# Performance work log

Measured on AMD Instinct MI355X. Metric: run time of the kernel, lower is better.

Reference implementation:

```python
import jax, jax.numpy as jnp
import numpy as np

B, N, M, C1, C2 = 4, 8192, 2048, 128, 256
H1, H2 = 256, 128  # mlp = [C2+C1, 256, 128]
EPS_DIST = 1e-8
EPS_BN = 1e-5
K = 3


def setup_inputs() -> dict:
    key = jax.random.key(0)
    ks = jax.random.split(key, 6)
    return {
        "unknown": jax.random.normal(ks[0], (B, N, 3), dtype=jnp.float32),
        "known": jax.random.normal(ks[1], (B, M, 3), dtype=jnp.float32),
        "unknow_feats": jax.random.normal(ks[2], (B, C1, N), dtype=jnp.float32),
        "known_feats": jax.random.normal(ks[3], (B, C2, M), dtype=jnp.float32),
        "W1": jax.random.normal(ks[4], (H1, C1 + C2), dtype=jnp.float32) * 0.05,
        "g1": jnp.ones((H1,), jnp.float32),
        "b1": jnp.zeros((H1,), jnp.float32),
        "W2": jax.random.normal(ks[5], (H2, H1), dtype=jnp.float32) * 0.05,
        "g2": jnp.ones((H2,), jnp.float32),
        "b2": jnp.zeros((H2,), jnp.float32),
    }


def _bn_relu(x, g, b):
    # training-mode BatchNorm over (batch, spatial) axes for (B, C, N) tensor
    mean = jnp.mean(x, axis=(0, 2), keepdims=True)
    var = jnp.var(x, axis=(0, 2), keepdims=True)
    y = (x - mean) * jax.lax.rsqrt(var + EPS_BN) * g[None, :, None] + b[None, :, None]
    return jax.nn.relu(y)


def reference(unknown, known, unknow_feats, known_feats, W1, g1, b1, W2, g2, b2):
    # 3-NN: squared euclidean distances (B, N, M) via expansion (avoids B,N,M,3 temp)
    d2 = (
        jnp.sum(unknown * unknown, axis=-1)[:, :, None]
        + jnp.sum(known * known, axis=-1)[:, None, :]
        - 2.0 * jnp.einsum("bnc,bmc->bnm", unknown, known)
    )
    neg_d, idx = jax.lax.top_k(-d2, K)  # smallest-K squared dists
    dist = -neg_d  # (B, N, K), squared distances (pytorch3d knn_points convention)
    recip = 1.0 / (dist + EPS_DIST)
    weight = recip / jnp.sum(recip, axis=2, keepdims=True)  # (B, N, K)

    kf = jnp.swapaxes(known_feats, 1, 2)  # (B, M, C2)
    grouped = jax.vmap(lambda f, i: f[i])(kf, idx)  # (B, N, K, C2)
    interp = jnp.einsum("bnkc,bnk->bcn", grouped, weight)  # (B, C2, N)

    x = jnp.concatenate([interp, unknow_feats], axis=1)  # (B, C2+C1, N)
    x = _bn_relu(jnp.einsum("oc,bcn->bon", W1, x), g1, b1)
    x = _bn_relu(jnp.einsum("oc,bcn->bon", W2, x), g2, b2)
    return x  # (B, H2, N)
```

## Files before the change

kernel.cpp:

```cpp
#include <hip/hip_runtime.h>
#include <hip/hip_bf16.h>
#include <cstdint>
#include <cstddef>

typedef unsigned short u16;
typedef __attribute__((ext_vector_type(8))) short bf16x8;
typedef __attribute__((ext_vector_type(4))) float f32x4;

constexpr int Bn = 4;
constexpr int Nq = 8192;
constexpr int Mk = 2048;
constexpr int C1c = 128;
constexpr int C2c = 256;
constexpr int H1c = 256;
constexpr int H2c = 128;

__device__ __forceinline__ float bf2f(u16 u) {
    union { uint32_t i; float f; } v;
    v.i = (uint32_t)u << 16;
    return v.f;
}
__device__ __forceinline__ u16 f2bf(float f) {
    const uint32_t x = __float_as_uint(f);
    return (u16)((x + 0x7FFFu + ((x >> 16) & 1u)) >> 16);
}
__device__ __forceinline__ uint32_t cvtpk(float lo, float hi) {
    uint32_t r;
    asm("v_cvt_pk_bf16_f32 %0, %1, %2" : "=v"(r) : "v"(lo), "v"(hi));
    return r;
}

__global__ __launch_bounds__(256) void knn_prep_kernel(
    const float* __restrict__ W1, const float* __restrict__ W2,
    u16* __restrict__ W1b, u16* __restrict__ W2b,
    const float* __restrict__ KF, u16* __restrict__ KFt,
    const float* __restrict__ UF, u16* __restrict__ UFt,
    const float* __restrict__ unknown, const float* __restrict__ known,
    int* __restrict__ idx_out, float* __restrict__ w_out)
{
    __shared__ __align__(16) char smem[32768];
    const int bid = blockIdx.x;
    const int t = threadIdx.x;

    if (bid < 1024) {
        float4* kp = (float4*)smem;
        const int b = bid >> 8;
        const int n0 = (bid & 255) * 32;

        const float* kb = known + (size_t)b * Mk * 3;
        for (int i = t; i < Mk; i += 256) {
            const float x = kb[i * 3 + 0], y = kb[i * 3 + 1], z = kb[i * 3 + 2];
            kp[i] = make_float4(x, y, z, fmaf(x, x, fmaf(y, y, z * z)));
        }
        __syncthreads();

        const int q = n0 + (t >> 3);
        const int s = t & 7;
        const float* u = unknown + ((size_t)b * Nq + q) * 3;
        const float ux = u[0], uy = u[1], uz = u[2];
        const float nux = -2.0f * ux, nuy = -2.0f * uy, nuz = -2.0f * uz;
        const float uu = fmaf(ux, ux, fmaf(uy, uy, uz * uz));

        float d0 = 1e30f, d1 = 1e30f, d2 = 1e30f;
        int i0 = 0, i1 = 0, i2 = 0;

        auto ins = [&](float d, int i) {
            const bool c0 = d < d0, c1 = d < d1, c2 = d < d2;
            const float nd0 = fminf(d0, d);
            const float nd1 = __builtin_amdgcn_fmed3f(d0, d, d1);
            const float nd2 = __builtin_amdgcn_fmed3f(d1, d, d2);
            i2 = c1 ? i1 : (c2 ? i : i2);
            i1 = c0 ? i0 : (c1 ? i : i1);
            i0 = c0 ? i : i0;
            d0 = nd0; d1 = nd1; d2 = nd2;
        };

        #pragma unroll 8
        for (int it = 0; it < Mk / 8; ++it) {
            const int m = it * 8 + s;
            const float4 p = kp[m];
            const float d = fmaf(nux, p.x, fmaf(nuy, p.y, fmaf(nuz, p.z, p.w)));
            ins(d, m);
        }
        #pragma unroll
        for (int off = 1; off <= 4; off <<= 1) {
            const float e0 = __shfl_xor(d0, off), e1 = __shfl_xor(d1, off), e2 = __shfl_xor(d2, off);
            const int j0 = __shfl_xor(i0, off), j1 = __shfl_xor(i1, off), j2 = __shfl_xor(i2, off);
            ins(e0, j0);
            ins(e1, j1);
            ins(e2, j2);
        }
        if (s == 0) {
            const float f0 = d0 + uu, f1 = d1 + uu, f2 = d2 + uu;
            const float r0 = 1.0f / (f0 + 1e-8f);
            const float r1 = 1.0f / (f1 + 1e-8f);
            const float r2 = 1.0f / (f2 + 1e-8f);
            const float inv = 1.0f / (r0 + r1 + r2);
            const size_t base = ((size_t)b * Nq + q) * 3;
            idx_out[base + 0] = i0;
            idx_out[base + 1] = i1;
            idx_out[base + 2] = i2;
            w_out[base + 0] = r0 * inv;
            w_out[base + 1] = r1 * inv;
            w_out[base + 2] = r2 * inv;
        }
    } else if (bid < 1152) {
        const int cb = bid - 1024;
        const float* X = (cb < 96) ? W1 : W2;
        u16* Y = (cb < 96) ? W1b : W2b;
        const int i = ((cb < 96) ? cb : (cb - 96)) * 256 + t;
        const float4 v = *(const float4*)&X[(size_t)i * 4];
        ushort4 o;
        o.x = f2bf(v.x); o.y = f2bf(v.y); o.z = f2bf(v.z); o.w = f2bf(v.w);
        *(ushort4*)&Y[(size_t)i * 4] = o;
    } else {
        const float* X;
        u16* Y;
        int C, M, m0, c0;
        if (bid < 1664) {
            const int f = bid - 1152;
            const int b = f >> 7, rem = f & 127;
            C = C2c; M = Mk; m0 = (rem >> 2) * 64; c0 = (rem & 3) * 64;
            X = KF + (size_t)b * C * M;
            Y = KFt + (size_t)b * M * C;
        } else {
            const int f = bid - 1664;
            const int b = f >> 8, rem = f & 255;
            C = C1c; M = Nq; m0 = (rem >> 1) * 64; c0 = (rem & 1) * 64;
            X = UF + (size_t)b * C * M;
            Y = UFt + (size_t)b * M * C;
        }
        float (*T)[65] = (float(*)[65])smem;
        const int m4 = (t & 15) * 4, cr = t >> 4;
        #pragma unroll
        for (int i = 0; i < 4; ++i) {
            const float4 v = *(const float4*)&X[(size_t)(c0 + cr + i * 16) * M + m0 + m4];
            T[cr + i * 16][m4 + 0] = v.x;
            T[cr + i * 16][m4 + 1] = v.y;
            T[cr + i * 16][m4 + 2] = v.z;
            T[cr + i * 16][m4 + 3] = v.w;
        }
        __syncthreads();
        const int c4 = (t & 15) * 4, mr = t >> 4;
        #pragma unroll
        for (int i = 0; i < 4; ++i) {
            const int m = mr + i * 16;
            ushort4 o;
            o.x = f2bf(T[c4 + 0][m]);
            o.y = f2bf(T[c4 + 1][m]);
            o.z = f2bf(T[c4 + 2][m]);
            o.w = f2bf(T[c4 + 3][m]);
            *(ushort4*)&Y[(size_t)(m0 + m) * C + c0 + c4] = o;
        }
    }
}

__device__ __forceinline__ uint4 bnx(uint4 x, const float* scs, const float* bis, int k) {
    const u16* p = (const u16*)&x;
    const float4 s0 = *(const float4*)&scs[k];
    const float4 s1 = *(const float4*)&scs[k + 4];
    const float4 b0 = *(const float4*)&bis[k];
    const float4 b1 = *(const float4*)&bis[k + 4];
    const float* sa = (const float*)&s0;
    const float* sb = (const float*)&s1;
    const float* ba = (const float*)&b0;
    const float* bb = (const float*)&b1;
    uint4 o;
    uint32_t* po = (uint32_t*)&o;
    #pragma unroll
    for (int w2 = 0; w2 < 2; ++w2) {
        const float a0 = fmaxf(0.0f, fmaf(bf2f(p[2 * w2 + 0]), sa[2 * w2 + 0], ba[2 * w2 + 0]));
        const float a1 = fmaxf(0.0f, fmaf(bf2f(p[2 * w2 + 1]), sa[2 * w2 + 1], ba[2 * w2 + 1]));
        po[w2] = cvtpk(a0, a1);
    }
    #pragma unroll
    for (int w2 = 0; w2 < 2; ++w2) {
        const float a0 = fmaxf(0.0f, fmaf(bf2f(p[4 + 2 * w2 + 0]), sb[2 * w2 + 0], bb[2 * w2 + 0]));
        const float a1 = fmaxf(0.0f, fmaf(bf2f(p[4 + 2 * w2 + 1]), sb[2 * w2 + 1], bb[2 * w2 + 1]));
        po[2 + w2] = cvtpk(a0, a1);
    }
    return o;
}

template <int GATHER, int STATS>
__global__ __launch_bounds__(256) void mfma_gemm(
    const u16* __restrict__ A, int lda, size_t sA,
    const u16* __restrict__ Bt, int ldb, size_t sB,
    u16* __restrict__ Cout, int ldc, size_t sC,
    int nK,
    const u16* __restrict__ Ptb,
    const int* __restrict__ idx, const float* __restrict__ wgt, int nrows,
    float* __restrict__ partS, float* __restrict__ partQ)
{
    __shared__ u16 As[4096];
    __shared__ u16 Bs[4096];
    __shared__ float sS[2][128], sQ[2][128];

    const int b = blockIdx.z;
    const int m0 = blockIdx.x * 128, n0 = blockIdx.y * 128;
    const int t = threadIdx.x;
    const int l = t & 63, wv = t >> 6;
    const int wr = wv >> 1, wc = wv & 1;

    const u16* Ab = A + (size_t)b * sA;
    const u16* Btb = Bt + (size_t)b * sB;
    const int rA0 = t >> 2, rA1 = (t + 256) >> 2;
    const int ko = (t & 3) * 8;

    f32x4 acc[4][4];
    const f32x4 z = {0.0f, 0.0f, 0.0f, 0.0f};
    #pragma unroll
    for (int i = 0; i < 4; ++i)
        #pragma unroll
        for (int j = 0; j < 4; ++j) acc[i][j] = z;

    uint4 a0 = *(const uint4*)&Ab[(size_t)(m0 + rA0) * lda + ko];
    uint4 a1 = *(const uint4*)&Ab[(size_t)(m0 + rA1) * lda + ko];
    uint4 b0 = *(const uint4*)&Btb[(size_t)(n0 + rA0) * ldb + ko];
    uint4 b1 = *(const uint4*)&Btb[(size_t)(n0 + rA1) * ldb + ko];

    for (int kt = 0; kt < nK; ++kt) {
        *(uint4*)&As[t * 8] = a0;
        *(uint4*)&As[(t + 256) * 8] = a1;
        *(uint4*)&Bs[t * 8] = b0;
        *(uint4*)&Bs[(t + 256) * 8] = b1;
        __syncthreads();
        if (kt + 1 < nK) {
            const int k0 = (kt + 1) * 32;
            a0 = *(const uint4*)&Ab[(size_t)(m0 + rA0) * lda + k0 + ko];
            a1 = *(const uint4*)&Ab[(size_t)(m0 + rA1) * lda + k0 + ko];
            b0 = *(const uint4*)&Btb[(size_t)(n0 + rA0) * ldb + k0 + ko];
            b1 = *(const uint4*)&Btb[(size_t)(n0 + rA1) * ldb + k0 + ko];
        }
        bf16x8 af[4], bf[4];
        #pragma unroll
        for (int f = 0; f < 4; ++f) {
            af[f] = *(const bf16x8*)&As[(wr * 64 + f * 16 + (l & 15)) * 32 + (l >> 4) * 8];
            bf[f] = *(const bf16x8*)&Bs[(wc * 64 + f * 16 + (l & 15)) * 32 + (l >> 4) * 8];
        }
        #pragma unroll
        for (int i = 0; i < 4; ++i)
            #pragma unroll
            for (int j = 0; j < 4; ++j)
                acc[i][j] = __builtin_amdgcn_mfma_f32_16x16x32_bf16(af[i], bf[j], acc[i][j], 0, 0, 0);
        __syncthreads();
    }

    const int cb = l & 15;
    const int rg = (l >> 4) * 4;
    float sj[4] = {0, 0, 0, 0}, qj[4] = {0, 0, 0, 0};
    #pragma unroll
    for (int i = 0; i < 4; ++i) {
        #pragma unroll
        for (int r = 0; r < 4; ++r) {
            const int R = m0 + wr * 64 + i * 16 + rg + r;
            const u16 *P0 = nullptr, *P1 = nullptr, *P2 = nullptr;
            float w0 = 0.0f, w1 = 0.0f, w2 = 0.0f;
            if (GATHER) {
                const size_t ib = ((size_t)b * nrows + R) * 3;
                const int j0 = idx[ib], j1 = idx[ib + 1], j2 = idx[ib + 2];
                w0 = wgt[ib];
                w1 = wgt[ib + 1];
                w2 = wgt[ib + 2];
                const u16* Pb = Ptb + (size_t)b * Mk * 256;
                P0 = Pb + (size_t)j0 * 256;
                P1 = Pb + (size_t)j1 * 256;
                P2 = Pb + (size_t)j2 * 256;
            }
            #pragma unroll
            for (int j = 0; j < 4; ++j) {
                const int Cc = n0 + wc * 64 + j * 16 + cb;
                float v = acc[i][j][r];
                if (GATHER)
                    v += w0 * bf2f(P0[Cc]) + w1 * bf2f(P1[Cc]) + w2 * bf2f(P2[Cc]);
                Cout[(size_t)b * sC + (size_t)R * ldc + Cc] = f2bf(v);
                if (STATS) {
                    sj[j] += v;
                    qj[j] += v * v;
                }
            }
        }
    }

    if (STATS) {
        #pragma unroll
        for (int j = 0; j < 4; ++j) {
            float s = sj[j], q = qj[j];
            s += __shfl_xor(s, 16); s += __shfl_xor(s, 32);
            q += __shfl_xor(q, 16); q += __shfl_xor(q, 32);
            if (l < 16) {
                sS[wr][wc * 64 + j * 16 + l] = s;
                sQ[wr][wc * 64 + j * 16 + l] = q;
            }
        }
        __syncthreads();
        if (t < 128) {
            const float S = sS[0][t] + sS[1][t];
            const float Q = sQ[0][t] + sQ[1][t];
            const int pblk = blockIdx.z * gridDim.x + blockIdx.x;
            partS[(size_t)pblk * 256 + blockIdx.y * 128 + t] = S;
            partQ[(size_t)pblk * 256 + blockIdx.y * 128 + t] = Q;
        }
    }
}

__global__ __launch_bounds__(256) void mfma_gemm3(
    const u16* __restrict__ W2b,
    const u16* __restrict__ Y,
    float* __restrict__ out,
    const float* __restrict__ bn_s, const float* __restrict__ bn_b,
    float* __restrict__ partS, float* __restrict__ partQ)
{
    __shared__ u16 As[2048];
    __shared__ u16 Bs[4096];
    __shared__ float scs[256], bis[256];
    __shared__ float sS[2][64], sQ[2][64];

    const int b = blockIdx.z;
    const int m0 = blockIdx.x * 64;
    const int n0 = blockIdx.y * 128;
    const int t = threadIdx.x;
    const int l = t & 63, wv = t >> 6;
    const int wr = wv >> 1, wc = wv & 1;

    scs[t] = bn_s[t];
    bis[t] = bn_b[t];

    const u16* Yb = Y + (size_t)b * Nq * 256;
    const int rA = t >> 2;
    const int rB1 = (t + 256) >> 2;
    const int ko = (t & 3) * 8;

    f32x4 acc[2][4];
    const f32x4 z = {0.0f, 0.0f, 0.0f, 0.0f};
    #pragma unroll
    for (int i = 0; i < 2; ++i)
        #pragma unroll
        for (int j = 0; j < 4; ++j) acc[i][j] = z;

    uint4 a0 = *(const uint4*)&W2b[(size_t)(m0 + rA) * 256 + ko];
    uint4 b0 = *(const uint4*)&Yb[(size_t)(n0 + rA) * 256 + ko];
    uint4 b1 = *(const uint4*)&Yb[(size_t)(n0 + rB1) * 256 + ko];
    __syncthreads();

    for (int kt = 0; kt < 8; ++kt) {
        const int k = kt * 32 + ko;
        *(uint4*)&As[t * 8] = a0;
        *(uint4*)&Bs[t * 8] = bnx(b0, scs, bis, k);
        *(uint4*)&Bs[(t + 256) * 8] = bnx(b1, scs, bis, k);
        __syncthreads();
        if (kt + 1 < 8) {
            const int k0 = (kt + 1) * 32;
            a0 = *(const uint4*)&W2b[(size_t)(m0 + rA) * 256 + k0 + ko];
            b0 = *(const uint4*)&Yb[(size_t)(n0 + rA) * 256 + k0 + ko];
            b1 = *(const uint4*)&Yb[(size_t)(n0 + rB1) * 256 + k0 + ko];
        }
        bf16x8 af[2], bf[4];
        #pragma unroll
        for (int f = 0; f < 2; ++f)
            af[f] = *(const bf16x8*)&As[(wr * 32 + f * 16 + (l & 15)) * 32 + (l >> 4) * 8];
        #pragma unroll
        for (int f = 0; f < 4; ++f)
            bf[f] = *(const bf16x8*)&Bs[(wc * 64 + f * 16 + (l & 15)) * 32 + (l >> 4) * 8];
        #pragma unroll
        for (int i = 0; i < 2; ++i)
            #pragma unroll
            for (int j = 0; j < 4; ++j)
                acc[i][j] = __builtin_amdgcn_mfma_f32_16x16x32_bf16(af[i], bf[j], acc[i][j], 0, 0, 0);
        __syncthreads();
    }

    const int cb = l & 15;
    const int rg = (l >> 4) * 4;
    float* ob = out + (size_t)b * H2c * Nq;
    #pragma unroll
    for (int i = 0; i < 2; ++i) {
        #pragma unroll
        for (int r = 0; r < 4; ++r) {
            const int Rl = wr * 32 + i * 16 + rg + r;
            #pragma unroll
            for (int j = 0; j < 4; ++j) {
                const int Cc = n0 + wc * 64 + j * 16 + cb;
                ob[(size_t)(m0 + Rl) * Nq + Cc] = acc[i][j][r];
            }
            float s = acc[i][0][r] + acc[i][1][r] + acc[i][2][r] + acc[i][3][r];
            float q = acc[i][0][r] * acc[i][0][r] + acc[i][1][r] * acc[i][1][r] +
                      acc[i][2][r] * acc[i][2][r] + acc[i][3][r] * acc[i][3][r];
            s += __shfl_xor(s, 1); s += __shfl_xor(s, 2);
            s += __shfl_xor(s, 4); s += __shfl_xor(s, 8);
            q += __shfl_xor(q, 1); q += __shfl_xor(q, 2);
            q += __shfl_xor(q, 4); q += __shfl_xor(q, 8);
            if ((l & 15) == 0) {
                sS[wc][Rl] = s;
                sQ[wc][Rl] = q;
            }
        }
    }
    __syncthreads();
    if (t < 64) {
        const float S = sS[0][t] + sS[1][t];
        const float Q = sQ[0][t] + sQ[1][t];
        const int p = blockIdx.z * gridDim.y + blockIdx.y;
        partS[(size_t)p * 128 + m0 + t] = S;
        partQ[(size_t)p * 128 + m0 + t] = Q;
    }
}

__global__ __launch_bounds__(1024) void bn_finalize(
    const float* __restrict__ pS, const float* __restrict__ pQ,
    const float* __restrict__ g, const float* __restrict__ beta,
    float* __restrict__ scale, float* __restrict__ bias,
    int C, int np, float cnt)
{
    __shared__ float rs[1024], rq[1024];
    const int t = threadIdx.x;
    const int c = t & (C - 1);
    const int sl = t / C;
    const int nsl = 1024 / C;
    float s = 0.0f, q = 0.0f;
    for (int i = sl; i < np; i += nsl) {
        s += pS[(size_t)i * C + c];
        q += pQ[(size_t)i * C + c];
    }
    rs[t] = s;
    rq[t] = q;
    __syncthreads();
    if (t < C) {
        for (int k = 1; k < nsl; ++k) {
            s += rs[t + k * C];
            q += rq[t + k * C];
        }
        const float mean = s / cnt;
        const float var = q / cnt - mean * mean;
        const float r = rsqrtf(var + 1e-5f);
        const float sc = g[t] * r;
        scale[t] = sc;
        bias[t] = beta[t] - mean * sc;
    }
}

__global__ __launch_bounds__(256) void bn2_apply_kernel(
    float* __restrict__ Y,
    const float* __restrict__ pS, const float* __restrict__ pQ,
    const float* __restrict__ g, const float* __restrict__ beta)
{
    __shared__ float rs[256], rq[256];
    const int t = threadIdx.x;
    const size_t base = (size_t)blockIdx.x * 1024;
    const int c = (int)((base / Nq) % H2c);

    rs[t] = pS[(size_t)t * 128 + c];
    rq[t] = pQ[(size_t)t * 128 + c];
    __syncthreads();
    for (int off = 128; off > 0; off >>= 1) {
        if (t < off) {
            rs[t] += rs[t + off];
            rq[t] += rq[t + off];
        }
        __syncthreads();
    }
    if (t == 0) {
        const float cnt = (float)(Bn * Nq);
        const float mean = rs[0] / cnt;
        const float var = rq[0] / cnt - mean * mean;
        const float r = rsqrtf(var + 1e-5f);
        const float sc = g[c] * r;
        rs[0] = sc;
        rq[0] = beta[c] - mean * sc;
    }
    __syncthreads();
    const float sc = rs[0], bi = rq[0];
    float4 v = *(float4*)&Y[base + t * 4];
    v.x = fmaxf(0.0f, fmaf(v.x, sc, bi));
    v.y = fmaxf(0.0f, fmaf(v.y, sc, bi));
    v.z = fmaxf(0.0f, fmaf(v.z, sc, bi));
    v.w = fmaxf(0.0f, fmaf(v.w, sc, bi));
    *(float4*)&Y[base + t * 4] = v;
}

extern "C" void kernel_launch(void* const* d_in, const int* in_sizes, int n_in,
                              void* d_out, int out_size, void* d_ws, size_t ws_size,
                              hipStream_t stream) {
    const float* unknown = (const float*)d_in[0];
    const float* known = (const float*)d_in[1];
    const float* unknow_feats = (const float*)d_in[2];
    const float* known_feats = (const float*)d_in[3];
    const float* W1 = (const float*)d_in[4];
    const float* g1 = (const float*)d_in[5];
    const float* b1 = (const float*)d_in[6];
    const float* W2 = (const float*)d_in[7];
    const float* g2 = (const float*)d_in[8];
    const float* b2 = (const float*)d_in[9];
    float* out = (float*)d_out;

    char* w = (char*)d_ws;
    u16* KFt = (u16*)w; w += (size_t)Bn * Mk * C2c * 2;
    u16* UFt = (u16*)w; w += (size_t)Bn * Nq * C1c * 2;
    u16* W1b = (u16*)w; w += (size_t)H1c * 384 * 2;
    u16* W2b = (u16*)w; w += (size_t)H2c * H1c * 2;
    u16* Ptb = (u16*)w; w += (size_t)Bn * Mk * H1c * 2;
    u16* y1b = (u16*)w; w += (size_t)Bn * Nq * H1c * 2;
    int* idx = (int*)w; w += (size_t)Bn * Nq * 3 * 4;
    float* wgt = (float*)w; w += (size_t)Bn * Nq * 3 * 4;
    float* pS1 = (float*)w; w += (size_t)256 * 256 * 4;
    float* pQ1 = (float*)w; w += (size_t)256 * 256 * 4;
    float* pS2 = (float*)w; w += (size_t)256 * 128 * 4;
    float* pQ2 = (float*)w; w += (size_t)256 * 128 * 4;
    float* scale1 = (float*)w; w += 1024;
    float* bias1 = (float*)w; w += 1024;

    knn_prep_kernel<<<2688, 256, 0, stream>>>(W1, W2, W1b, W2b,
                                              known_feats, KFt, unknow_feats, UFt,
                                              unknown, known, idx, wgt);

    mfma_gemm<0, 0><<<dim3(Mk / 128, H1c / 128, Bn), 256, 0, stream>>>(
        KFt, C2c, (size_t)Mk * C2c,
        W1b, 384, 0,
        Ptb, H1c, (size_t)Mk * H1c,
        C2c / 32, nullptr, nullptr, nullptr, 0, nullptr, nullptr);

    mfma_gemm<1, 1><<<dim3(Nq / 128, H1c / 128, Bn), 256, 0, stream>>>(
        UFt, C1c, (size_t)Nq * C1c,
        W1b + C2c, 384, 0,
        y1b, H1c, (size_t)Nq * H1c,
        C1c / 32, Ptb, idx, wgt, Nq, pS1, pQ1);

    bn_finalize<<<1, 1024, 0, stream>>>(pS1, pQ1, g1, b1, scale1, bias1,
                                        H1c, 256, (float)(Bn * Nq));

    mfma_gemm3<<<dim3(2, Nq / 128, Bn), 256, 0, stream>>>(
        W2b, y1b, out, scale1, bias1, pS2, pQ2);

    bn2_apply_kernel<<<(Bn * H2c * Nq) / 1024, 256, 0, stream>>>(out, pS2, pQ2, g2, b2);
}
```

Baseline: 104.8 us.

## Fuse known-feature projection GEMM into prep kernel and BN1 finalize into GEMM2

The known-feature GEMM (KF^T times W1[:, :256]) now runs inside the prep kernel: each block reads fp32 known_feats and W1, converts them to bf16 while staging in LDS, and writes the projected Ptb directly. This removes the KFt transpose buffer and one kernel launch. The BN1 finalize kernel is also removed. The last block of the second GEMM, detected with an atomic counter, reduces the partial sums and writes scale/bias. Launch count and intermediate traffic go down, at the cost of a smaller 64x64 MFMA tile with no overlap between loads and MMA, and a serial 256-step reduction in a single block.

Result: slower. 166.7 us (+59.0%).

```diff
diff --git a/kernel.cpp b/kernel.cpp
--- a/kernel.cpp
+++ b/kernel.cpp
@@ -33,10 +33,11 @@
 __global__ __launch_bounds__(256) void knn_prep_kernel(
     const float* __restrict__ W1, const float* __restrict__ W2,
     u16* __restrict__ W1b, u16* __restrict__ W2b,
-    const float* __restrict__ KF, u16* __restrict__ KFt,
+    const float* __restrict__ KF, u16* __restrict__ Ptb,
     const float* __restrict__ UF, u16* __restrict__ UFt,
     const float* __restrict__ unknown, const float* __restrict__ known,
-    int* __restrict__ idx_out, float* __restrict__ w_out)
+    int* __restrict__ idx_out, float* __restrict__ w_out,
+    int* __restrict__ done1)
 {
     __shared__ __align__(16) char smem[32768];
     const int bid = blockIdx.x;
@@ -105,6 +106,7 @@
             w_out[base + 2] = r2 * inv;
         }
     } else if (bid < 1152) {
+        if (bid == 1024 && t == 0) *done1 = 0;
         const int cb = bid - 1024;
         const float* X = (cb < 96) ? W1 : W2;
         u16* Y = (cb < 96) ? W1b : W2b;
@@ -113,28 +115,88 @@
         ushort4 o;
         o.x = f2bf(v.x); o.y = f2bf(v.y); o.z = f2bf(v.z); o.w = f2bf(v.w);
         *(ushort4*)&Y[(size_t)i * 4] = o;
+    } else if (bid < 1664) {
+        u16* As = (u16*)smem;
+        u16* Bs = (u16*)(smem + 5120);
+        const int f = bid - 1152;
+        const int b = f >> 7;
+        const int rem = f & 127;
+        const int m0 = (rem >> 2) * 64;
+        const int h0 = (rem & 3) * 64;
+        const float* KFb = KF + (size_t)b * C2c * Mk;
+        const int l = t & 63, wv = t >> 6;
+        const int wr = wv >> 1, wc = wv & 1;
+
+        f32x4 acc[2][2];
+        const f32x4 z = {0.0f, 0.0f, 0.0f, 0.0f};
+        acc[0][0] = z; acc[0][1] = z; acc[1][0] = z; acc[1][1] = z;
+
+        const int cA = t >> 3;
+        const int mcA = (t & 7) * 8;
+        const int hB = t >> 2;
+        const int khB = (t & 3) * 8;
+
+        for (int kt = 0; kt < 8; ++kt) {
+            const int kc = kt * 32;
+            {
+                const float* src = &KFb[(size_t)(kc + cA) * Mk + m0 + mcA];
+                const float4 v0 = *(const float4*)&src[0];
+                const float4 v1 = *(const float4*)&src[4];
+                As[(mcA + 0) * 40 + cA] = f2bf(v0.x);
+                As[(mcA + 1) * 40 + cA] = f2bf(v0.y);
+                As[(mcA + 2) * 40 + cA] = f2bf(v0.z);
+                As[(mcA + 3) * 40 + cA] = f2bf(v0.w);
+                As[(mcA + 4) * 40 + cA] = f2bf(v1.x);
+                As[(mcA + 5) * 40 + cA] = f2bf(v1.y);
+                As[(mcA + 6) * 40 + cA] = f2bf(v1.z);
+                As[(mcA + 7) * 40 + cA] = f2bf(v1.w);
+            }
+            {
+                const float* src = &W1[(size_t)(h0 + hB) * 384 + kc + khB];
+                const float4 v0 = *(const float4*)&src[0];
+                const float4 v1 = *(const float4*)&src[4];
+                u16 o[8] = {f2bf(v0.x), f2bf(v0.y), f2bf(v0.z), f2bf(v0.w),
+                            f2bf(v1.x), f2bf(v1.y), f2bf(v1.z), f2bf(v1.w)};
+                *(uint4*)&Bs[hB * 40 + khB] = *(const uint4*)o;
+            }
+            __syncthreads();
+            bf16x8 af[2], bf[2];
+            #pragma unroll
+            for (int ff = 0; ff < 2; ++ff) {
+                af[ff] = *(const bf16x8*)&As[(wr * 32 + ff * 16 + (l & 15)) * 40 + (l >> 4) * 8];
+                bf[ff] = *(const bf16x8*)&Bs[(wc * 32 + ff * 16 + (l & 15)) * 40 + (l >> 4) * 8];
+            }
+            #pragma unroll
+            for (int i = 0; i < 2; ++i)
+                #pragma unroll
+                for (int j = 0; j < 2; ++j)
+                    acc[i][j] = __builtin_amdgcn_mfma_f32_16x16x32_bf16(af[i], bf[j], acc[i][j], 0, 0, 0);
+            __syncthreads();
+        }
+
+        u16* Pb = Ptb + (size_t)b * Mk * 256;
+        const int cb = l & 15, rg = (l >> 4) * 4;
+        #pragma unroll
+        for (int i = 0; i < 2; ++i) {
+            #pragma unroll
+            for (int r = 0; r < 4; ++r) {
+                const int row = m0 + wr * 32 + i * 16 + rg + r;
+                #pragma unroll
+                for (int j = 0; j < 2; ++j)
+                    Pb[(size_t)row * 256 + h0 + wc * 32 + j * 16 + cb] = f2bf(acc[i][j][r]);
+            }
+        }
     } else {
-        const float* X;
-        u16* Y;
-        int C, M, m0, c0;
-        if (bid < 1664) {
-            const int f = bid - 1152;
-            const int b = f >> 7, rem = f & 127;
-            C = C2c; M = Mk; m0 = (rem >> 2) * 64; c0 = (rem & 3) * 64;
-            X = KF + (size_t)b * C * M;
-            Y = KFt + (size_t)b * M * C;
-        } else {
-            const int f = bid - 1664;
-            const int b = f >> 8, rem = f & 255;
-            C = C1c; M = Nq; m0 = (rem >> 1) * 64; c0 = (rem & 1) * 64;
-            X = UF + (size_t)b * C * M;
-            Y = UFt + (size_t)b * M * C;
-        }
+        const int f = bid - 1664;
+        const int b = f >> 8, rem = f & 255;
+        const int m0 = (rem >> 1) * 64, c0 = (rem & 1) * 64;
+        const float* X = UF + (size_t)b * C1c * Nq;
+        u16* Y = UFt + (size_t)b * Nq * C1c;
         float (*T)[65] = (float(*)[65])smem;
         const int m4 = (t & 15) * 4, cr = t >> 4;
         #pragma unroll
         for (int i = 0; i < 4; ++i) {
-            const float4 v = *(const float4*)&X[(size_t)(c0 + cr + i * 16) * M + m0 + m4];
+            const float4 v = *(const float4*)&X[(size_t)(c0 + cr + i * 16) * Nq + m0 + m4];
             T[cr + i * 16][m4 + 0] = v.x;
             T[cr + i * 16][m4 + 1] = v.y;
             T[cr + i * 16][m4 + 2] = v.z;
@@ -150,8 +212,141 @@
             o.y = f2bf(T[c4 + 1][m]);
             o.z = f2bf(T[c4 + 2][m]);
             o.w = f2bf(T[c4 + 3][m]);
-            *(ushort4*)&Y[(size_t)(m0 + m) * C + c0 + c4] = o;
-        }
+            *(ushort4*)&Y[(size_t)(m0 + m) * C1c + c0 + c4] = o;
+        }
+    }
+}
+
+__global__ __launch_bounds__(256) void mfma_gemm2(
+    const u16* __restrict__ A,
+    const u16* __restrict__ Bt,
+    u16* __restrict__ Cout,
+    const u16* __restrict__ Ptb,
+    const int* __restrict__ idx, const float* __restrict__ wgt,
+    float* __restrict__ partS, float* __restrict__ partQ,
+    const float* __restrict__ g1, const float* __restrict__ b1g,
+    float* __restrict__ scale1, float* __restrict__ bias1,
+    int* __restrict__ done1)
+{
+    __shared__ u16 As[4096];
+    __shared__ u16 Bs[4096];
+    __shared__ float sS[2][128], sQ[2][128];
+    __shared__ int lastFlag;
+
+    const int b = blockIdx.z;
+    const int m0 = blockIdx.x * 128, n0 = blockIdx.y * 128;
+    const int t = threadIdx.x;
+    const int l = t & 63, wv = t >> 6;
+    const int wr = wv >> 1, wc = wv & 1;
+
+    const u16* Ab = A + (size_t)b * Nq * C1c;
+    const int rA0 = t >> 2, rA1 = (t + 256) >> 2;
+    const int ko = (t & 3) * 8;
+
+    f32x4 acc[4][4];
+    const f32x4 z = {0.0f, 0.0f, 0.0f, 0.0f};
+    #pragma unroll
+    for (int i = 0; i < 4; ++i)
+        #pragma unroll
+        for (int j = 0; j < 4; ++j) acc[i][j] = z;
+
+    uint4 a0 = *(const uint4*)&Ab[(size_t)(m0 + rA0) * C1c + ko];
+    uint4 a1 = *(const uint4*)&Ab[(size_t)(m0 + rA1) * C1c + ko];
+    uint4 b0 = *(const uint4*)&Bt[(size_t)(n0 + rA0) * 384 + ko];
+    uint4 b1 = *(const uint4*)&Bt[(size_t)(n0 + rA1) * 384 + ko];
+
+    for (int kt = 0; kt < C1c / 32; ++kt) {
+        *(uint4*)&As[t * 8] = a0;
+        *(uint4*)&As[(t + 256) * 8] = a1;
+        *(uint4*)&Bs[t * 8] = b0;
+        *(uint4*)&Bs[(t + 256) * 8] = b1;
+        __syncthreads();
+        if (kt + 1 < C1c / 32) {
+            const int k0 = (kt + 1) * 32;
+            a0 = *(const uint4*)&Ab[(size_t)(m0 + rA0) * C1c + k0 + ko];
+            a1 = *(const uint4*)&Ab[(size_t)(m0 + rA1) * C1c + k0 + ko];
+            b0 = *(const uint4*)&Bt[(size_t)(n0 + rA0) * 384 + k0 + ko];
+            b1 = *(const uint4*)&Bt[(size_t)(n0 + rA1) * 384 + k0 + ko];
+        }
+        bf16x8 af[4], bf[4];
+        #pragma unroll
+        for (int f = 0; f < 4; ++f) {
+            af[f] = *(const bf16x8*)&As[(wr * 64 + f * 16 + (l & 15)) * 32 + (l >> 4) * 8];
+            bf[f] = *(const bf16x8*)&Bs[(wc * 64 + f * 16 + (l & 15)) * 32 + (l >> 4) * 8];
+        }
+        #pragma unroll
+        for (int i = 0; i < 4; ++i)
+            #pragma unroll
+            for (int j = 0; j < 4; ++j)
+                acc[i][j] = __builtin_amdgcn_mfma_f32_16x16x32_bf16(af[i], bf[j], acc[i][j], 0, 0, 0);
+        __syncthreads();
+    }
+
+    const int cb = l & 15;
+    const int rg = (l >> 4) * 4;
+    float sj[4] = {0, 0, 0, 0}, qj[4] = {0, 0, 0, 0};
+    #pragma unroll
+    for (int i = 0; i < 4; ++i) {
+        #pragma unroll
+        for (int r = 0; r < 4; ++r) {
+            const int R = m0 + wr * 64 + i * 16 + rg + r;
+            const size_t ib = ((size_t)b * Nq + R) * 3;
+            const int j0 = idx[ib], j1 = idx[ib + 1], j2 = idx[ib + 2];
+            const float w0 = wgt[ib], w1 = wgt[ib + 1], w2 = wgt[ib + 2];
+            const u16* Pb = Ptb + (size_t)b * Mk * 256;
+            const u16* P0 = Pb + (size_t)j0 * 256;
+            const u16* P1 = Pb + (size_t)j1 * 256;
+            const u16* P2 = Pb + (size_t)j2 * 256;
+            #pragma unroll
+            for (int j = 0; j < 4; ++j) {
+                const int Cc = n0 + wc * 64 + j * 16 + cb;
+                float v = acc[i][j][r];
+                v += w0 * bf2f(P0[Cc]) + w1 * bf2f(P1[Cc]) + w2 * bf2f(P2[Cc]);
+                Cout[(size_t)b * Nq * 256 + (size_t)R * 256 + Cc] = f2bf(v);
+                sj[j] += v;
+                qj[j] += v * v;
+            }
+        }
+    }
+
+    #pragma unroll
+    for (int j = 0; j < 4; ++j) {
+        float s = sj[j], q = qj[j];
+        s += __shfl_xor(s, 16); s += __shfl_xor(s, 32);
+        q += __shfl_xor(q, 16); q += __shfl_xor(q, 32);
+        if (l < 16) {
+            sS[wr][wc * 64 + j * 16 + l] = s;
+            sQ[wr][wc * 64 + j * 16 + l] = q;
+        }
+    }
+    __syncthreads();
+    if (t < 128) {
+        const float S = sS[0][t] + sS[1][t];
+        const float Q = sQ[0][t] + sQ[1][t];
+        const int pblk = blockIdx.z * gridDim.x + blockIdx.x;
+        partS[(size_t)pblk * 256 + blockIdx.y * 128 + t] = S;
+        partQ[(size_t)pblk * 256 + blockIdx.y * 128 + t] = Q;
+    }
+
+    __syncthreads();
+    __threadfence();
+    if (t == 0) lastFlag = (atomicAdd(done1, 1) == 511);
+    __syncthreads();
+    if (lastFlag) {
+        __threadfence();
+        float s = 0.0f, q = 0.0f;
+        #pragma unroll 4
+        for (int p = 0; p < 256; ++p) {
+            s += partS[(size_t)p * 256 + t];
+            q += partQ[(size_t)p * 256 + t];
+        }
+        const float cnt = (float)(Bn * Nq);
+        const float mean = s / cnt;
+        const float var = q / cnt - mean * mean;
+        const float rv = rsqrtf(var + 1e-5f);
+        const float sc = g1[t] * rv;
+        scale1[t] = sc;
+        bias1[t] = b1g[t] - mean * sc;
     }
 }
 
@@ -182,128 +377,6 @@
     return o;
 }
 
-template <int GATHER, int STATS>
-__global__ __launch_bounds__(256) void mfma_gemm(
-    const u16* __restrict__ A, int lda, size_t sA,
-    const u16* __restrict__ Bt, int ldb, size_t sB,
-    u16* __restrict__ Cout, int ldc, size_t sC,
-    int nK,
-    const u16* __restrict__ Ptb,
-    const int* __restrict__ idx, const float* __restrict__ wgt, int nrows,
-    float* __restrict__ partS, float* __restrict__ partQ)
-{
-    __shared__ u16 As[4096];
-    __shared__ u16 Bs[4096];
-    __shared__ float sS[2][128], sQ[2][128];
-
-    const int b = blockIdx.z;
-    const int m0 = blockIdx.x * 128, n0 = blockIdx.y * 128;
-    const int t = threadIdx.x;
-    const int l = t & 63, wv = t >> 6;
-    const int wr = wv >> 1, wc = wv & 1;
-
-    const u16* Ab = A + (size_t)b * sA;
-    const u16* Btb = Bt + (size_t)b * sB;
-    const int rA0 = t >> 2, rA1 = (t + 256) >> 2;
-    const int ko = (t & 3) * 8;
-
-    f32x4 acc[4][4];
-    const f32x4 z = {0.0f, 0.0f, 0.0f, 0.0f};
-    #pragma unroll
-    for (int i = 0; i < 4; ++i)
-        #pragma unroll
-        for (int j = 0; j < 4; ++j) acc[i][j] = z;
-
-    uint4 a0 = *(const uint4*)&Ab[(size_t)(m0 + rA0) * lda + ko];
-    uint4 a1 = *(const uint4*)&Ab[(size_t)(m0 + rA1) * lda + ko];
-    uint4 b0 = *(const uint4*)&Btb[(size_t)(n0 + rA0) * ldb + ko];
-    uint4 b1 = *(const uint4*)&Btb[(size_t)(n0 + rA1) * ldb + ko];
-
-    for (int kt = 0; kt < nK; ++kt) {
-        *(uint4*)&As[t * 8] = a0;
-        *(uint4*)&As[(t + 256) * 8] = a1;
-        *(uint4*)&Bs[t * 8] = b0;
-        *(uint4*)&Bs[(t + 256) * 8] = b1;
-        __syncthreads();
-        if (kt + 1 < nK) {
-            const int k0 = (kt + 1) * 32;
-            a0 = *(const uint4*)&Ab[(size_t)(m0 + rA0) * lda + k0 + ko];
-            a1 = *(const uint4*)&Ab[(size_t)(m0 + rA1) * lda + k0 + ko];
-            b0 = *(const uint4*)&Btb[(size_t)(n0 + rA0) * ldb + k0 + ko];
-            b1 = *(const uint4*)&Btb[(size_t)(n0 + rA1) * ldb + k0 + ko];
-        }
-        bf16x8 af[4], bf[4];
-        #pragma unroll
-        for (int f = 0; f < 4; ++f) {
-            af[f] = *(const bf16x8*)&As[(wr * 64 + f * 16 + (l & 15)) * 32 + (l >> 4) * 8];
-            bf[f] = *(const bf16x8*)&Bs[(wc * 64 + f * 16 + (l & 15)) * 32 + (l >> 4) * 8];
-        }
-        #pragma unroll
-        for (int i = 0; i < 4; ++i)
-            #pragma unroll
-            for (int j = 0; j < 4; ++j)
-                acc[i][j] = __builtin_amdgcn_mfma_f32_16x16x32_bf16(af[i], bf[j], acc[i][j], 0, 0, 0);
-        __syncthreads();
-    }
-
-    const int cb = l & 15;
-    const int rg = (l >> 4) * 4;
-    float sj[4] = {0, 0, 0, 0}, qj[4] = {0, 0, 0, 0};
-    #pragma unroll
-    for (int i = 0; i < 4; ++i) {
-        #pragma unroll
-        for (int r = 0; r < 4; ++r) {
-            const int R = m0 + wr * 64 + i * 16 + rg + r;
-            const u16 *P0 = nullptr, *P1 = nullptr, *P2 = nullptr;
-            float w0 = 0.0f, w1 = 0.0f, w2 = 0.0f;
-            if (GATHER) {
-                const size_t ib = ((size_t)b * nrows + R) * 3;
-                const int j0 = idx[ib], j1 = idx[ib + 1], j2 = idx[ib + 2];
-                w0 = wgt[ib];
-                w1 = wgt[ib + 1];
-                w2 = wgt[ib + 2];
-                const u16* Pb = Ptb + (size_t)b * Mk * 256;
-                P0 = Pb + (size_t)j0 * 256;
-                P1 = Pb + (size_t)j1 * 256;
-                P2 = Pb + (size_t)j2 * 256;
-            }
-            #pragma unroll
-            for (int j = 0; j < 4; ++j) {
-                const int Cc = n0 + wc * 64 + j * 16 + cb;
-                float v = acc[i][j][r];
-                if (GATHER)
-                    v += w0 * bf2f(P0[Cc]) + w1 * bf2f(P1[Cc]) + w2 * bf2f(P2[Cc]);
-                Cout[(size_t)b * sC + (size_t)R * ldc + Cc] = f2bf(v);
-                if (STATS) {
-                    sj[j] += v;
-                    qj[j] += v * v;
-                }
-            }
-        }
-    }
-
-    if (STATS) {
-        #pragma unroll
-        for (int j = 0; j < 4; ++j) {
-            float s = sj[j], q = qj[j];
-            s += __shfl_xor(s, 16); s += __shfl_xor(s, 32);
-            q += __shfl_xor(q, 16); q += __shfl_xor(q, 32);
-            if (l < 16) {
-                sS[wr][wc * 64 + j * 16 + l] = s;
-                sQ[wr][wc * 64 + j * 16 + l] = q;
-            }
-        }
-        __syncthreads();
-        if (t < 128) {
-            const float S = sS[0][t] + sS[1][t];
-            const float Q = sQ[0][t] + sQ[1][t];
-            const int pblk = blockIdx.z * gridDim.x + blockIdx.x;
-            partS[(size_t)pblk * 256 + blockIdx.y * 128 + t] = S;
-            partQ[(size_t)pblk * 256 + blockIdx.y * 128 + t] = Q;
-        }
-    }
-}
-
 __global__ __launch_bounds__(256) void mfma_gemm3(
     const u16* __restrict__ W2b,
     const u16* __restrict__ Y,
@@ -403,39 +476,6 @@
         const int p = blockIdx.z * gridDim.y + blockIdx.y;
         partS[(size_t)p * 128 + m0 + t] = S;
         partQ[(size_t)p * 128 + m0 + t] = Q;
-    }
-}
-
-__global__ __launch_bounds__(1024) void bn_finalize(
-    const float* __restrict__ pS, const float* __restrict__ pQ,
-    const float* __restrict__ g, const float* __restrict__ beta,
-    float* __restrict__ scale, float* __restrict__ bias,
-    int C, int np, float cnt)
-{
-    __shared__ float rs[1024], rq[1024];
-    const int t = threadIdx.x;
-    const int c = t & (C - 1);
-    const int sl = t / C;
-    const int nsl = 1024 / C;
-    float s = 0.0f, q = 0.0f;
-    for (int i = sl; i < np; i += nsl) {
-        s += pS[(size_t)i * C + c];
-        q += pQ[(size_t)i * C + c];
-    }
-    rs[t] = s;
-    rq[t] = q;
-    __syncthreads();
-    if (t < C) {
-        for (int k = 1; k < nsl; ++k) {
-            s += rs[t + k * C];
-            q += rq[t + k * C];
-        }
-        const float mean = s / cnt;
-        const float var = q / cnt - mean * mean;
-        const float r = rsqrtf(var + 1e-5f);
-        const float sc = g[t] * r;
-        scale[t] = sc;
-        bias[t] = beta[t] - mean * sc;
     }
 }
 
@@ -494,7 +534,6 @@
     float* out = (float*)d_out;
 
     char* w = (char*)d_ws;
-    u16* KFt = (u16*)w; w += (size_t)Bn * Mk * C2c * 2;
     u16* UFt = (u16*)w; w += (size_t)Bn * Nq * C1c * 2;
     u16* W1b = (u16*)w; w += (size_t)H1c * 384 * 2;
     u16* W2b = (u16*)w; w += (size_t)H2c * H1c * 2;
@@ -508,25 +547,15 @@
     float* pQ2 = (float*)w; w += (size_t)256 * 128 * 4;
     float* scale1 = (float*)w; w += 1024;
     float* bias1 = (float*)w; w += 1024;
+    int* done1 = (int*)w; w += 1024;
 
     knn_prep_kernel<<<2688, 256, 0, stream>>>(W1, W2, W1b, W2b,
-                                              known_feats, KFt, unknow_feats, UFt,
-                                              unknown, known, idx, wgt);
-
-    mfma_gemm<0, 0><<<dim3(Mk / 128, H1c / 128, Bn), 256, 0, stream>>>(
-        KFt, C2c, (size_t)Mk * C2c,
-        W1b, 384, 0,
-        Ptb, H1c, (size_t)Mk * H1c,
-        C2c / 32, nullptr, nullptr, nullptr, 0, nullptr, nullptr);
-
-    mfma_gemm<1, 1><<<dim3(Nq / 128, H1c / 128, Bn), 256, 0, stream>>>(
-        UFt, C1c, (size_t)Nq * C1c,
-        W1b + C2c, 384, 0,
-        y1b, H1c, (size_t)Nq * H1c,
-        C1c / 32, Ptb, idx, wgt, Nq, pS1, pQ1);
-
-    bn_finalize<<<1, 1024, 0, stream>>>(pS1, pQ1, g1, b1, scale1, bias1,
-                                        H1c, 256, (float)(Bn * Nq));
+                                              known_feats, Ptb, unknow_feats, UFt,
+                                              unknown, known, idx, wgt, done1);
+
+    mfma_gemm2<<<dim3(Nq / 128, H1c / 128, Bn), 256, 0, stream>>>(
+        UFt, W1b + C2c, y1b, Ptb, idx, wgt, pS1, pQ1,
+        g1, b1, scale1, bias1, done1);
 
     mfma_gemm3<<<dim3(2, Nq / 128, Bn), 256, 0, stream>>>(
         W2b, y1b, out, scale1, bias1, pS2, pQ2);
```
